# Optimization experiments

Hardware: AMD Instinct MI355X
Metric: run time of the kernel (lower is better)

## Reference

```python
import jax, jax.numpy as jnp
import numpy as np

IN_DIM, HID, D_PK = 6, 64, 64
B, T = 256, 2048
EPS = 1e-5


def setup_inputs() -> dict:
    key = jax.random.key(0)
    ks = jax.random.split(key, 12)
    s_in = 1.0 / np.sqrt(IN_DIM)
    s_h = 1.0 / np.sqrt(HID)
    return {
        "drug_ce": jax.random.normal(ks[0], (B, T, IN_DIM), dtype=jnp.float32),
        "w1": jax.random.uniform(ks[1], (IN_DIM, HID), minval=-s_in, maxval=s_in, dtype=jnp.float32),
        "b1": jax.random.uniform(ks[2], (HID,), minval=-s_in, maxval=s_in, dtype=jnp.float32),
        "ln1_g": jnp.ones((HID,), jnp.float32),
        "ln1_b": jnp.zeros((HID,), jnp.float32),
        "W_ih": jax.random.uniform(ks[3], (3 * HID, HID), minval=-s_h, maxval=s_h, dtype=jnp.float32),
        "b_ih": jax.random.uniform(ks[4], (3 * HID,), minval=-s_h, maxval=s_h, dtype=jnp.float32),
        "W_hh": jax.random.uniform(ks[5], (3 * HID, HID), minval=-s_h, maxval=s_h, dtype=jnp.float32),
        "b_hh": jax.random.uniform(ks[6], (3 * HID,), minval=-s_h, maxval=s_h, dtype=jnp.float32),
        "w2": jax.random.uniform(ks[7], (HID, D_PK), minval=-s_h, maxval=s_h, dtype=jnp.float32),
        "b2": jax.random.uniform(ks[8], (D_PK,), minval=-s_h, maxval=s_h, dtype=jnp.float32),
        "ln2_g": jnp.ones((D_PK,), jnp.float32),
        "ln2_b": jnp.zeros((D_PK,), jnp.float32),
    }


def _layernorm(x, g, b):
    m = jnp.mean(x, axis=-1, keepdims=True)
    v = jnp.mean(jnp.square(x - m), axis=-1, keepdims=True)
    return (x - m) * jax.lax.rsqrt(v + EPS) * g + b


def reference(drug_ce, w1, b1, ln1_g, ln1_b, W_ih, b_ih, W_hh, b_hh, w2, b2, ln2_g, ln2_b):
    # input_proj: Linear -> LayerNorm -> GELU (exact, erf-based as in torch)
    x = jax.nn.gelu(_layernorm(drug_ce @ w1 + b1, ln1_g, ln1_b), approximate=False)  # (B,T,H)

    # Precompute input-side gate pre-activations for all timesteps
    gi = jnp.einsum('bth,gh->btg', x, W_ih) + b_ih  # (B,T,3H)
    gi_t = jnp.swapaxes(gi, 0, 1)  # (T,B,3H)

    h0 = jnp.zeros((drug_ce.shape[0], HID), dtype=drug_ce.dtype)

    def step(h, gi_step):
        gh = h @ W_hh.T + b_hh  # (B,3H)
        i_r, i_z, i_n = jnp.split(gi_step, 3, axis=-1)
        h_r, h_z, h_n = jnp.split(gh, 3, axis=-1)
        r = jax.nn.sigmoid(i_r + h_r)
        z = jax.nn.sigmoid(i_z + h_z)
        n = jnp.tanh(i_n + r * h_n)
        h_new = (1.0 - z) * n + z * h
        return h_new, h_new

    _, h_seq_t = jax.lax.scan(step, h0, gi_t)  # (T,B,H)
    h_seq = jnp.swapaxes(h_seq_t, 0, 1)  # (B,T,H)

    # out_proj: Linear -> LayerNorm
    return _layernorm(h_seq @ w2 + b2, ln2_g, ln2_b)
```

## Files before the change

kernel.cpp:

```cpp
#include <hip/hip_runtime.h>
#include <math.h>

#define HID 64
#define TST 2048
#define CH 16
#define NCH (TST / CH)
#define EPSN 1e-5f

typedef float v2f __attribute__((ext_vector_type(2)));

#define REP32(M) M(0) M(1) M(2) M(3) M(4) M(5) M(6) M(7) \
                 M(8) M(9) M(10) M(11) M(12) M(13) M(14) M(15) \
                 M(16) M(17) M(18) M(19) M(20) M(21) M(22) M(23) \
                 M(24) M(25) M(26) M(27) M(28) M(29) M(30) M(31)

__global__ void k_inproj(const float* __restrict__ ce, const float* __restrict__ w1,
                         const float* __restrict__ b1, const float* __restrict__ g1,
                         const float* __restrict__ be1, float* __restrict__ xout,
                         int nrows) {
    const int lane = threadIdx.x & 63;
    const int wave = threadIdx.x >> 6;
    const long row = (long)blockIdx.x * 4 + wave;
    if (row >= nrows) return;
    const float* cr = ce + row * 6;
    float acc = b1[lane];
    acc += cr[0] * w1[0 * HID + lane];
    acc += cr[1] * w1[1 * HID + lane];
    acc += cr[2] * w1[2 * HID + lane];
    acc += cr[3] * w1[3 * HID + lane];
    acc += cr[4] * w1[4 * HID + lane];
    acc += cr[5] * w1[5 * HID + lane];
    float s = acc;
#pragma unroll
    for (int m = 32; m >= 1; m >>= 1) s += __shfl_xor(s, m, 64);
    const float mean = s * (1.0f / 64.0f);
    const float d = acc - mean;
    float q = d * d;
#pragma unroll
    for (int m = 32; m >= 1; m >>= 1) q += __shfl_xor(q, m, 64);
    const float var = q * (1.0f / 64.0f);
    const float xn = d * rsqrtf(var + EPSN) * g1[lane] + be1[lane];
    const float ge = 0.5f * xn * (1.0f + erff(xn * 0.70710678118654752440f));
    xout[row * HID + lane] = ge;
}

__global__ __launch_bounds__(256, 1)
__attribute__((amdgpu_waves_per_eu(1, 1)))
void k_gru(float* xo,
           const float* __restrict__ W_ih, const float* __restrict__ b_ih,
           const float* __restrict__ W_hh, const float* __restrict__ b_hh,
           const float* __restrict__ w2, const float* __restrict__ b2,
           const float* __restrict__ g2, const float* __restrict__ be2) {
    __shared__ __align__(16) float4 xbuf[2][CH][16];
    __shared__ __align__(16) float gibuf[2][CH][192];
    __shared__ __align__(16) float hist[2][CH][HID];
    __shared__ __align__(16) float hbuf[HID];

    const int tid = threadIdx.x;
    const int lane = tid & 63;
    const int wv = tid >> 6;
    float* xb = xo + (size_t)blockIdx.x * TST * HID;

#define DECLW(i) v2f A##i = {0.f, 0.f}, B##i = {0.f, 0.f}, C##i = {0.f, 0.f};
    REP32(DECLW)
    float sc0 = 0.f, sc1 = 0.f, sc2 = 0.f;

    if (wv == 0) {
        const v2f* r0 = (const v2f*)(W_hh + (size_t)lane * HID);
        const v2f* r1 = (const v2f*)(W_hh + (size_t)(64 + lane) * HID);
        const v2f* r2 = (const v2f*)(W_hh + (size_t)(128 + lane) * HID);
#define LW0(i) A##i = r0[i]; B##i = r1[i]; C##i = r2[i];
        REP32(LW0)
        sc0 = b_hh[lane]; sc1 = b_hh[64 + lane]; sc2 = b_hh[128 + lane];
        hbuf[lane] = 0.0f;
    } else if (wv == 1) {
        const v2f* rA = (const v2f*)(W_ih + (size_t)lane * HID);
        const v2f* rB = (const v2f*)(W_ih + (size_t)(128 + lane) * HID);
#define LW1(i) A##i = rA[i]; B##i = rB[i];
        REP32(LW1)
        sc0 = b_ih[lane]; sc1 = b_ih[128 + lane];
    } else if (wv == 2) {
        const v2f* rC = (const v2f*)(W_ih + (size_t)(64 + lane) * HID);
#define LW2(i) A##i = rC[i];
        REP32(LW2)
        sc0 = b_ih[64 + lane];
    } else {
#define LW3(i) A##i.x = w2[(size_t)(2 * (i)) * HID + lane]; \
               A##i.y = w2[(size_t)(2 * (i) + 1) * HID + lane];
        REP32(LW3)
        sc0 = b2[lane]; sc1 = g2[lane]; sc2 = be2[lane];
    }

#define PINW(i) asm volatile("" : "+v"(A##i), "+v"(B##i), "+v"(C##i));
    REP32(PINW)

    {
        const float4* src = (const float4*)xb;
        ((float4*)xbuf[0])[tid] = src[tid];
    }
    float h_reg = 0.0f;
    __syncthreads();

    for (int p = 0; p <= NCH + 1; ++p) {
        if (wv == 0) {
            if (p >= 1 && p <= NCH) {
                const int c = p - 1;
                const float* gp = (const float*)gibuf[c & 1];
                float* hp = (float*)hist[c & 1];
                for (int t = 0; t < CH; ++t) {
                    const float gr = gp[t * 192 + lane];
                    const float gz = gp[t * 192 + 64 + lane];
                    const float gn = gp[t * 192 + 128 + lane];
                    const v2f* hv = (const v2f*)hbuf;
                    v2f ar0 = {0.f, 0.f}, ar1 = {0.f, 0.f};
                    v2f az0 = {0.f, 0.f}, az1 = {0.f, 0.f};
                    v2f an0 = {0.f, 0.f}, an1 = {0.f, 0.f};
#define SFMA(i) { const v2f h2 = hv[i]; \
                  if ((i) & 1) { ar1 += A##i * h2; az1 += B##i * h2; an1 += C##i * h2; } \
                  else         { ar0 += A##i * h2; az0 += B##i * h2; an0 += C##i * h2; } }
                    REP32(SFMA)
                    const v2f arv = ar0 + ar1;
                    const v2f azv = az0 + az1;
                    const v2f anv = an0 + an1;
                    const float rpre = gr + arv.x + arv.y + sc0;
                    const float zpre = gz + azv.x + azv.y + sc1;
                    const float hn = anv.x + anv.y + sc2;
                    const float r = 1.0f / (1.0f + __expf(-rpre));
                    const float z = 1.0f / (1.0f + __expf(-zpre));
                    const float pre = gn + r * hn;
                    const float e2 = __expf(2.0f * pre);
                    const float n = 1.0f - 2.0f / (e2 + 1.0f);
                    h_reg = (1.0f - z) * n + z * h_reg;
                    hbuf[lane] = h_reg;
                    hp[t * HID + lane] = h_reg;
                }
            }
        } else if (wv == 1 || wv == 2) {
            if (p < NCH) {
                const float4* xc = (const float4*)xbuf[p & 1];
                float* gp = (float*)gibuf[p & 1];
                for (int t = 0; t < CH; ++t) {
                    const v2f* xv = (const v2f*)(xc + t * 16);
                    v2f aA0 = {0.f, 0.f}, aA1 = {0.f, 0.f};
                    v2f aB0 = {0.f, 0.f}, aB1 = {0.f, 0.f};
                    if (wv == 1) {
#define GFMA1(i) { const v2f x2 = xv[i]; \
                   if ((i) & 1) { aA1 += A##i * x2; aB1 += B##i * x2; } \
                   else         { aA0 += A##i * x2; aB0 += B##i * x2; } }
                        REP32(GFMA1)
                        gp[t * 192 + lane] = aA0.x + aA0.y + aA1.x + aA1.y + sc0;
                        gp[t * 192 + 128 + lane] = aB0.x + aB0.y + aB1.x + aB1.y + sc1;
                    } else {
#define GFMA2(i) { const v2f x2 = xv[i]; \
                   if ((i) & 1) { aA1 += A##i * x2; } \
                   else         { aA0 += A##i * x2; } }
                        REP32(GFMA2)
                        gp[t * 192 + 64 + lane] = aA0.x + aA0.y + aA1.x + aA1.y + sc0;
                    }
                }
            }
        } else {
            if (p >= 2) {
                const int ce = p - 2;
                const float* hp = (const float*)hist[ce & 1];
#pragma unroll
                for (int half = 0; half < 2; ++half) {
                    float yv[8], sv[8], qv[8];
#pragma unroll
                    for (int u = 0; u < 8; ++u) {
                        const int t = half * 8 + u;
                        const v2f* hr = (const v2f*)(hp + t * HID);
                        v2f a20 = {0.f, 0.f}, a21 = {0.f, 0.f};
#define EFMA(i) { const v2f h2 = hr[i]; \
                  if ((i) & 1) { a21 += A##i * h2; } else { a20 += A##i * h2; } }
                        REP32(EFMA)
                        yv[u] = sc0 + a20.x + a20.y + a21.x + a21.y;
                    }
#pragma unroll
                    for (int u = 0; u < 8; ++u) { sv[u] = yv[u]; qv[u] = yv[u] * yv[u]; }
#pragma unroll
                    for (int m = 32; m >= 1; m >>= 1) {
#pragma unroll
                        for (int u = 0; u < 8; ++u) sv[u] += __shfl_xor(sv[u], m, 64);
#pragma unroll
                        for (int u = 0; u < 8; ++u) qv[u] += __shfl_xor(qv[u], m, 64);
                    }
#pragma unroll
                    for (int u = 0; u < 8; ++u) {
                        const int t = half * 8 + u;
                        const float mean = sv[u] * (1.0f / 64.0f);
                        const float var = qv[u] * (1.0f / 64.0f) - mean * mean;
                        const float dd = yv[u] - mean;
                        xb[(size_t)(ce * CH + t) * HID + lane] =
                            dd * rsqrtf(var + EPSN) * sc1 + sc2;
                    }
                }
            }
            if (p + 1 < NCH) {
                const float4* src = (const float4*)(xb + (size_t)(p + 1) * CH * HID);
                float4* dst = (float4*)xbuf[(p + 1) & 1];
#pragma unroll
                for (int q2 = 0; q2 < 4; ++q2) dst[lane + q2 * 64] = src[lane + q2 * 64];
            }
        }
        __syncthreads();
    }
}

extern "C" void kernel_launch(void* const* d_in, const int* in_sizes, int n_in,
                              void* d_out, int out_size, void* d_ws, size_t ws_size,
                              hipStream_t stream) {
    const float* ce  = (const float*)d_in[0];
    const float* w1  = (const float*)d_in[1];
    const float* b1  = (const float*)d_in[2];
    const float* g1  = (const float*)d_in[3];
    const float* be1 = (const float*)d_in[4];
    const float* Wih = (const float*)d_in[5];
    const float* bih = (const float*)d_in[6];
    const float* Whh = (const float*)d_in[7];
    const float* bhh = (const float*)d_in[8];
    const float* w2  = (const float*)d_in[9];
    const float* b2  = (const float*)d_in[10];
    const float* g2  = (const float*)d_in[11];
    const float* be2 = (const float*)d_in[12];
    float* out = (float*)d_out;

    const int nrows = in_sizes[0] / 6;
    const int B = nrows / TST;

    k_inproj<<<(nrows + 3) / 4, 256, 0, stream>>>(ce, w1, b1, g1, be1, out, nrows);
    k_gru<<<B, 256, 0, stream>>>(out, Wih, bih, Whh, bhh, w2, b2, g2, be2);
}
```

Measured before the change: 1.802 ms.

## Split GRU recurrence across three waves with per-step barrier and partial exchange

The recurrent matvec, previously done by a single wave computing all three gates, is split across three waves, one per gate row-block. Each wave recomputes the GRU nonlinearity redundantly and exchanges its gate pre-activations through shared memory every timestep. The block grows to 8 waves (512 threads) with launch bounds allowing 2 blocks per CU, and input projection, output projection/LayerNorm and prefetch are rescheduled to a per-timestep pipeline. This shortens the serial dependency chain per step at the cost of a __syncthreads every timestep instead of every 16-step chunk.

```diff
diff --git a/kernel.cpp b/kernel.cpp
--- a/kernel.cpp
+++ b/kernel.cpp
@@ -44,8 +44,17 @@
     xout[row * HID + lane] = ge;
 }
 
-__global__ __launch_bounds__(256, 1)
-__attribute__((amdgpu_waves_per_eu(1, 1)))
+__device__ __forceinline__ float gru_step(float gr, float gz, float gn,
+                                          float pr, float pz, float pn, float h) {
+    const float r = 1.0f / (1.0f + __expf(-(gr + pr)));
+    const float z = 1.0f / (1.0f + __expf(-(gz + pz)));
+    const float pre = gn + r * pn;
+    const float e2 = __expf(2.0f * pre);
+    const float n = 1.0f - 2.0f / (e2 + 1.0f);
+    return (1.0f - z) * n + z * h;
+}
+
+__global__ __launch_bounds__(512, 2)
 void k_gru(float* xo,
            const float* __restrict__ W_ih, const float* __restrict__ b_ih,
            const float* __restrict__ W_hh, const float* __restrict__ b_hh,
@@ -53,154 +62,119 @@
            const float* __restrict__ g2, const float* __restrict__ be2) {
     __shared__ __align__(16) float4 xbuf[2][CH][16];
     __shared__ __align__(16) float gibuf[2][CH][192];
-    __shared__ __align__(16) float hist[2][CH][HID];
-    __shared__ __align__(16) float hbuf[HID];
+    __shared__ __align__(16) float hist[4][CH][HID];
+    __shared__ __align__(16) float hb[3][HID];
+    __shared__ __align__(16) float part[2][3][HID];
+    __shared__ __align__(16) float ybuf[2][8][HID];
 
     const int tid = threadIdx.x;
     const int lane = tid & 63;
     const int wv = tid >> 6;
     float* xb = xo + (size_t)blockIdx.x * TST * HID;
 
-#define DECLW(i) v2f A##i = {0.f, 0.f}, B##i = {0.f, 0.f}, C##i = {0.f, 0.f};
+#define DECLW(i) v2f W##i = {0.f, 0.f};
     REP32(DECLW)
-    float sc0 = 0.f, sc1 = 0.f, sc2 = 0.f;
-
-    if (wv == 0) {
-        const v2f* r0 = (const v2f*)(W_hh + (size_t)lane * HID);
-        const v2f* r1 = (const v2f*)(W_hh + (size_t)(64 + lane) * HID);
-        const v2f* r2 = (const v2f*)(W_hh + (size_t)(128 + lane) * HID);
-#define LW0(i) A##i = r0[i]; B##i = r1[i]; C##i = r2[i];
-        REP32(LW0)
-        sc0 = b_hh[lane]; sc1 = b_hh[64 + lane]; sc2 = b_hh[128 + lane];
-        hbuf[lane] = 0.0f;
-    } else if (wv == 1) {
-        const v2f* rA = (const v2f*)(W_ih + (size_t)lane * HID);
-        const v2f* rB = (const v2f*)(W_ih + (size_t)(128 + lane) * HID);
-#define LW1(i) A##i = rA[i]; B##i = rB[i];
-        REP32(LW1)
-        sc0 = b_ih[lane]; sc1 = b_ih[128 + lane];
-    } else if (wv == 2) {
-        const v2f* rC = (const v2f*)(W_ih + (size_t)(64 + lane) * HID);
-#define LW2(i) A##i = rC[i];
-        REP32(LW2)
-        sc0 = b_ih[64 + lane];
-    } else {
-#define LW3(i) A##i.x = w2[(size_t)(2 * (i)) * HID + lane]; \
-               A##i.y = w2[(size_t)(2 * (i) + 1) * HID + lane];
-        REP32(LW3)
-        sc0 = b2[lane]; sc1 = g2[lane]; sc2 = be2[lane];
+    float bh = 0.f, b2r = 0.f, g2r = 0.f, be2r = 0.f;
+
+    if (wv < 6) {
+        const float* wbp = (wv < 3) ? (W_hh + (size_t)(wv * 64 + lane) * HID)
+                                    : (W_ih + (size_t)((wv - 3) * 64 + lane) * HID);
+        const v2f* r0 = (const v2f*)wbp;
+#define LWR(i) W##i = r0[i];
+        REP32(LWR)
+        bh = (wv < 3) ? b_hh[wv * 64 + lane] : b_ih[(wv - 3) * 64 + lane];
+    } else if (wv == 6) {
+#define LW6(i) W##i.x = w2[(size_t)(2 * (i)) * HID + lane]; \
+               W##i.y = w2[(size_t)(2 * (i) + 1) * HID + lane];
+        REP32(LW6)
+        b2r = b2[lane]; g2r = g2[lane]; be2r = be2[lane];
     }
-
-#define PINW(i) asm volatile("" : "+v"(A##i), "+v"(B##i), "+v"(C##i));
+#define PINW(i) asm volatile("" : "+v"(W##i));
     REP32(PINW)
 
-    {
-        const float4* src = (const float4*)xb;
-        ((float4*)xbuf[0])[tid] = src[tid];
-    }
-    float h_reg = 0.0f;
+    if (tid < 256) ((float4*)&xbuf[0][0][0])[tid] = ((const float4*)xb)[tid];
+    if (wv < 3) part[0][wv][lane] = bh;
+    float h_reg = 0.f;
+    float pown = bh;
     __syncthreads();
 
-    for (int p = 0; p <= NCH + 1; ++p) {
-        if (wv == 0) {
-            if (p >= 1 && p <= NCH) {
-                const int c = p - 1;
-                const float* gp = (const float*)gibuf[c & 1];
-                float* hp = (float*)hist[c & 1];
-                for (int t = 0; t < CH; ++t) {
-                    const float gr = gp[t * 192 + lane];
-                    const float gz = gp[t * 192 + 64 + lane];
-                    const float gn = gp[t * 192 + 128 + lane];
-                    const v2f* hv = (const v2f*)hbuf;
-                    v2f ar0 = {0.f, 0.f}, ar1 = {0.f, 0.f};
-                    v2f az0 = {0.f, 0.f}, az1 = {0.f, 0.f};
-                    v2f an0 = {0.f, 0.f}, an1 = {0.f, 0.f};
-#define SFMA(i) { const v2f h2 = hv[i]; \
-                  if ((i) & 1) { ar1 += A##i * h2; az1 += B##i * h2; an1 += C##i * h2; } \
-                  else         { ar0 += A##i * h2; az0 += B##i * h2; an0 += C##i * h2; } }
-                    REP32(SFMA)
-                    const v2f arv = ar0 + ar1;
-                    const v2f azv = az0 + az1;
-                    const v2f anv = an0 + an1;
-                    const float rpre = gr + arv.x + arv.y + sc0;
-                    const float zpre = gz + azv.x + azv.y + sc1;
-                    const float hn = anv.x + anv.y + sc2;
-                    const float r = 1.0f / (1.0f + __expf(-rpre));
-                    const float z = 1.0f / (1.0f + __expf(-zpre));
-                    const float pre = gn + r * hn;
-                    const float e2 = __expf(2.0f * pre);
-                    const float n = 1.0f - 2.0f / (e2 + 1.0f);
-                    h_reg = (1.0f - z) * n + z * h_reg;
-                    hbuf[lane] = h_reg;
-                    hp[t * HID + lane] = h_reg;
-                }
-            }
-        } else if (wv == 1 || wv == 2) {
-            if (p < NCH) {
-                const float4* xc = (const float4*)xbuf[p & 1];
-                float* gp = (float*)gibuf[p & 1];
-                for (int t = 0; t < CH; ++t) {
-                    const v2f* xv = (const v2f*)(xc + t * 16);
-                    v2f aA0 = {0.f, 0.f}, aA1 = {0.f, 0.f};
-                    v2f aB0 = {0.f, 0.f}, aB1 = {0.f, 0.f};
-                    if (wv == 1) {
-#define GFMA1(i) { const v2f x2 = xv[i]; \
-                   if ((i) & 1) { aA1 += A##i * x2; aB1 += B##i * x2; } \
-                   else         { aA0 += A##i * x2; aB0 += B##i * x2; } }
-                        REP32(GFMA1)
-                        gp[t * 192 + lane] = aA0.x + aA0.y + aA1.x + aA1.y + sc0;
-                        gp[t * 192 + 128 + lane] = aB0.x + aB0.y + aB1.x + aB1.y + sc1;
-                    } else {
-#define GFMA2(i) { const v2f x2 = xv[i]; \
-                   if ((i) & 1) { aA1 += A##i * x2; } \
-                   else         { aA0 += A##i * x2; } }
-                        REP32(GFMA2)
-                        gp[t * 192 + 64 + lane] = aA0.x + aA0.y + aA1.x + aA1.y + sc0;
-                    }
-                }
+#define MACH(i) { const v2f u = hv[i]; if ((i) & 1) a1 += W##i * u; else a0 += W##i * u; }
+#define MACX(i) { const v2f u = xv[i]; if ((i) & 1) a1 += W##i * u; else a0 += W##i * u; }
+#define MACE(i) { const v2f u = hr[i]; if ((i) & 1) a1 += W##i * u; else a0 += W##i * u; }
+
+#define LNR4(slot, ub, chk, rbase) { \
+    float yv[4], sv[4], qv[4]; \
+    _Pragma("unroll") for (int u = 0; u < 4; ++u) yv[u] = ybuf[slot][(ub) + u][lane]; \
+    _Pragma("unroll") for (int u = 0; u < 4; ++u) { sv[u] = yv[u]; qv[u] = yv[u] * yv[u]; } \
+    _Pragma("unroll") for (int m = 32; m >= 1; m >>= 1) { \
+        _Pragma("unroll") for (int u = 0; u < 4; ++u) sv[u] += __shfl_xor(sv[u], m, 64); \
+        _Pragma("unroll") for (int u = 0; u < 4; ++u) qv[u] += __shfl_xor(qv[u], m, 64); } \
+    _Pragma("unroll") for (int u = 0; u < 4; ++u) { \
+        const float mean = sv[u] * (1.0f / 64.0f); \
+        const float var = qv[u] * (1.0f / 64.0f) - mean * mean; \
+        const float dd = yv[u] - mean; \
+        xb[(size_t)((chk) * CH + (rbase) + u) * HID + lane] = \
+            dd * rsqrtf(var + EPSN) * g2r + be2r; } }
+
+    for (int s = -16; s <= 2081; ++s) {
+        const int c = s >> 4;
+        const int t = s & 15;
+        if (wv < 3) {
+            if (s >= 0 && s < TST) {
+                const float* gp = &gibuf[c & 1][t][0];
+                const float gr = gp[lane], gz = gp[64 + lane], gn = gp[128 + lane];
+                float pr, pz, pn;
+                if (wv == 0)      { pr = pown;                   pz = part[s & 1][1][lane]; pn = part[s & 1][2][lane]; }
+                else if (wv == 1) { pr = part[s & 1][0][lane];   pz = pown;                 pn = part[s & 1][2][lane]; }
+                else              { pr = part[s & 1][0][lane];   pz = part[s & 1][1][lane]; pn = pown; }
+                h_reg = gru_step(gr, gz, gn, pr, pz, pn, h_reg);
+                hb[wv][lane] = h_reg;
+                const v2f* hv = (const v2f*)&hb[wv][0];
+                v2f a0 = {0.f, 0.f}, a1 = {0.f, 0.f};
+                REP32(MACH)
+                const v2f av = a0 + a1;
+                pown = av.x + av.y + bh;
+                part[(s + 1) & 1][wv][lane] = pown;
+            }
+        } else if (wv < 6) {
+            if (s < TST - CH) {
+                const int sf = s + CH;
+                const v2f* xv = (const v2f*)&xbuf[(sf >> 4) & 1][sf & 15][0];
+                v2f a0 = {0.f, 0.f}, a1 = {0.f, 0.f};
+                REP32(MACX)
+                const v2f av = a0 + a1;
+                gibuf[(sf >> 4) & 1][sf & 15][(wv - 3) * 64 + lane] = av.x + av.y + bh;
+            }
+        } else if (wv == 6) {
+            if (s >= 32 && c <= 129) {
+                const v2f* hr = (const v2f*)&hist[(c - 2) & 3][t][0];
+                v2f a0 = {0.f, 0.f}, a1 = {0.f, 0.f};
+                REP32(MACE)
+                const v2f av = a0 + a1;
+                ybuf[t >> 3][t & 7][lane] = b2r + av.x + av.y;
+            }
+            if ((t == 8 || t == 9) && c >= 2 && c <= 129) {
+                const int ub = (t - 8) * 4;
+                LNR4(0, ub, c - 2, ub)
+            }
+            if ((t == 0 || t == 1) && c >= 3 && c <= 130) {
+                const int ub = t * 4;
+                LNR4(1, ub, c - 3, 8 + ub)
             }
         } else {
-            if (p >= 2) {
-                const int ce = p - 2;
-                const float* hp = (const float*)hist[ce & 1];
+            if (s >= 0 && s < TST) {
+                const float* gp = &gibuf[c & 1][t][0];
+                const float pr = part[s & 1][0][lane];
+                const float pz = part[s & 1][1][lane];
+                const float pn = part[s & 1][2][lane];
+                h_reg = gru_step(gp[lane], gp[64 + lane], gp[128 + lane], pr, pz, pn, h_reg);
+                hist[c & 3][t][lane] = h_reg;
+            }
+            if (t == 0 && c >= -1 && c <= 125) {
+                const float4* src = (const float4*)(xb + (size_t)(c + 2) * CH * HID);
+                float4* dst = (float4*)&xbuf[c & 1][0][0];
 #pragma unroll
-                for (int half = 0; half < 2; ++half) {
-                    float yv[8], sv[8], qv[8];
-#pragma unroll
-                    for (int u = 0; u < 8; ++u) {
-                        const int t = half * 8 + u;
-                        const v2f* hr = (const v2f*)(hp + t * HID);
-                        v2f a20 = {0.f, 0.f}, a21 = {0.f, 0.f};
-#define EFMA(i) { const v2f h2 = hr[i]; \
-                  if ((i) & 1) { a21 += A##i * h2; } else { a20 += A##i * h2; } }
-                        REP32(EFMA)
-                        yv[u] = sc0 + a20.x + a20.y + a21.x + a21.y;
-                    }
-#pragma unroll
-                    for (int u = 0; u < 8; ++u) { sv[u] = yv[u]; qv[u] = yv[u] * yv[u]; }
-#pragma unroll
-                    for (int m = 32; m >= 1; m >>= 1) {
-#pragma unroll
-                        for (int u = 0; u < 8; ++u) sv[u] += __shfl_xor(sv[u], m, 64);
-#pragma unroll
-                        for (int u = 0; u < 8; ++u) qv[u] += __shfl_xor(qv[u], m, 64);
-                    }
-#pragma unroll
-                    for (int u = 0; u < 8; ++u) {
-                        const int t = half * 8 + u;
-                        const float mean = sv[u] * (1.0f / 64.0f);
-                        const float var = qv[u] * (1.0f / 64.0f) - mean * mean;
-                        const float dd = yv[u] - mean;
-                        xb[(size_t)(ce * CH + t) * HID + lane] =
-                            dd * rsqrtf(var + EPSN) * sc1 + sc2;
-                    }
-                }
-            }
-            if (p + 1 < NCH) {
-                const float4* src = (const float4*)(xb + (size_t)(p + 1) * CH * HID);
-                float4* dst = (float4*)xbuf[(p + 1) & 1];
-#pragma unroll
-                for (int q2 = 0; q2 < 4; ++q2) dst[lane + q2 * 64] = src[lane + q2 * 64];
+                for (int q = 0; q < 4; ++q) dst[lane + q * 64] = src[lane + q * 64];
             }
         }
         __syncthreads();
@@ -229,5 +203,5 @@
     const int B = nrows / TST;
 
     k_inproj<<<(nrows + 3) / 4, 256, 0, stream>>>(ce, w1, b1, g1, be1, out, nrows);
-    k_gru<<<B, 256, 0, stream>>>(out, Wih, bih, Whh, bhh, w2, b2, g2, be2);
-}
+    k_gru<<<B, 512, 0, stream>>>(out, Wih, bih, Whh, bhh, w2, b2, g2, be2);
+}
```

Result: no change. 1.785 ms (-0.9%).
